# Kernel optimization log

Measured on AMD Instinct MI355X. Metric: run time of the kernel, lower is better.

## Reference

```python
import jax, jax.numpy as jnp
import numpy as np

B, N, C, H = 4, 1024, 256, 8
HD = C // H
SCALE = HD ** -0.5


def setup_inputs() -> dict:
    key = jax.random.key(0)
    ks = jax.random.split(key, 8)
    x = jax.random.normal(ks[0], (B, N, C), jnp.float32)
    voxel_coord = jax.random.uniform(ks[1], (B, N, 3), jnp.float32)
    # Linear weights stored as [in, out] so y = x @ W + b (same math as torch x @ W.T)
    W_qk = jax.random.normal(ks[2], (C, 2 * C), jnp.float32) * 0.02
    W_v = jax.random.normal(ks[3], (C, C), jnp.float32) * 0.02
    W_proj = jax.random.normal(ks[4], (C, C), jnp.float32) * 0.02
    b_proj = jnp.zeros((C,), jnp.float32)
    W_pos = jax.random.normal(ks[5], (4, H), jnp.float32) * 0.02
    b_pos = jnp.zeros((H,), jnp.float32)
    gating = jnp.ones((H,), jnp.float32)
    return dict(x=x, voxel_coord=voxel_coord, W_qk=W_qk, W_v=W_v,
                W_proj=W_proj, b_proj=b_proj, W_pos=W_pos, b_pos=b_pos,
                gating=gating)


def reference(x, voxel_coord, W_qk, W_v, W_proj, b_proj, W_pos, b_pos, gating):
    b, n, c = x.shape
    # Relative 3D positional encoding: positions[b,i,j] = p[j] - p[i]; feature = [dx,dy,dz,dist]
    diff = voxel_coord[:, None, :, :] - voxel_coord[:, :, None, :]          # [B,N,N,3]
    dist = jnp.sqrt(jnp.sum(diff * diff, axis=-1, keepdims=True))           # [B,N,N,1]
    rel = jnp.concatenate([diff, dist], axis=-1)                            # [B,N,N,4]

    # Positional score per head, softmax over keys j
    pos_logits = jnp.einsum('bijf,fh->bhij', rel, W_pos) + b_pos[None, :, None, None]
    pos_score = jax.nn.softmax(pos_logits, axis=-1)                         # [B,H,N,N]

    # Content score: SDPA with V = I  ==  plain softmax attention matrix
    qk = (x @ W_qk).reshape(b, n, 2, H, HD)
    q = jnp.transpose(qk[:, :, 0], (0, 2, 1, 3))                            # [B,H,N,hd]
    k = jnp.transpose(qk[:, :, 1], (0, 2, 1, 3))
    patch_score = jax.nn.softmax(jnp.einsum('bhid,bhjd->bhij', q, k) * SCALE, axis=-1)

    # Gated mix + renormalize
    sig = jax.nn.sigmoid(gating)[None, :, None, None]
    attn = (1.0 - sig) * patch_score + sig * pos_score
    attn = attn / jnp.sum(attn, axis=-1, keepdims=True)

    v = (x @ W_v).reshape(b, n, H, HD).transpose(0, 2, 1, 3)                # [B,H,N,hd]
    out = jnp.einsum('bhij,bhjd->bihd', attn, v).reshape(b, n, c)           # [B,N,C]
    out = out @ W_proj + b_proj
    return out
```

## Files before the change

### kernel.cpp

```cpp
#include <hip/hip_runtime.h>
#include <hip/hip_bf16.h>

#define LOG2E 1.4426950408889634f

typedef __attribute__((ext_vector_type(8))) short bf16x8_t;
typedef __attribute__((ext_vector_type(4))) float f32x4_t;

#if __has_builtin(__builtin_amdgcn_exp2f)
#define EXP2F_(x) __builtin_amdgcn_exp2f(x)
#else
__device__ __forceinline__ float EXP2F_(float x) {
    float r; asm volatile("v_exp_f32 %0, %1\ns_nop 1" : "=v"(r) : "v"(x)); return r;
}
#endif
#if __has_builtin(__builtin_amdgcn_sqrtf)
#define SQRTF_(x) __builtin_amdgcn_sqrtf(x)
#else
__device__ __forceinline__ float SQRTF_(float x) {
    float r; asm volatile("v_sqrt_f32 %0, %1\ns_nop 1" : "=v"(r) : "v"(x)); return r;
}
#endif

__device__ __forceinline__ unsigned short f2bf(float f) {
    unsigned u = __float_as_uint(f);
    u += 0x7fffu + ((u >> 16) & 1u);
    return (unsigned short)(u >> 16);
}

__device__ __forceinline__ unsigned pk2(float lo, float hi) {
    union { __hip_bfloat162 h2; unsigned u; } cvt;
    cvt.h2 = __float22bfloat162_rn(make_float2(lo, hi));
    return cvt.u;
}

__device__ __forceinline__ void stage16(const void* g, void* l, int lane) {
#if __has_builtin(__builtin_amdgcn_global_load_lds)
    __builtin_amdgcn_global_load_lds((const __attribute__((address_space(1))) void*)g,
                                     (__attribute__((address_space(3))) void*)l, 16, 0, 0);
#else
    *(uint4*)((char*)l + lane * 16) = *(const uint4*)g;
#endif
}

__global__ __launch_bounds__(256) void k_convert(
    const float* __restrict__ Wqk, const float* __restrict__ Wv,
    const float* __restrict__ Wpj, const float* __restrict__ coords,
    const float* __restrict__ W_pos,
    unsigned short* __restrict__ Wqk_t, unsigned short* __restrict__ Wv_t,
    unsigned short* __restrict__ Wp_t, float4* __restrict__ tbl)
{
    __shared__ unsigned short T[64 * 72];
    const int bid = blockIdx.x, tid = threadIdx.x;
    if (bid < 64) {
        const float* src; unsigned short* dst; int N_, kt, nt;
        if (bid < 32)      { src = Wqk; dst = Wqk_t; N_ = 512; kt = bid & 3; nt = bid >> 2; }
        else if (bid < 48) { int t = bid - 32; src = Wv;  dst = Wv_t; N_ = 256; kt = t & 3; nt = t >> 2; }
        else               { int t = bid - 48; src = Wpj; dst = Wp_t; N_ = 256; kt = t & 3; nt = t >> 2; }
        const int kr = tid >> 2, seg = tid & 3;
        #pragma unroll
        for (int u = 0; u < 4; ++u) {
            float4 v = *(const float4*)(src + (kt * 64 + kr) * N_ + nt * 64 + seg * 16 + u * 4);
            T[(seg * 16 + u * 4 + 0) * 72 + kr] = f2bf(v.x);
            T[(seg * 16 + u * 4 + 1) * 72 + kr] = f2bf(v.y);
            T[(seg * 16 + u * 4 + 2) * 72 + kr] = f2bf(v.z);
            T[(seg * 16 + u * 4 + 3) * 72 + kr] = f2bf(v.w);
        }
        __syncthreads();
        const int n = tid >> 2, s2 = tid & 3;
        uint4 a = *(uint4*)&T[n * 72 + s2 * 16];
        uint4 b2 = *(uint4*)&T[n * 72 + s2 * 16 + 8];
        *(uint4*)(dst + (nt * 64 + n) * 256 + kt * 64 + s2 * 16) = a;
        *(uint4*)(dst + (nt * 64 + n) * 256 + kt * 64 + s2 * 16 + 8) = b2;
    } else {
        const int bh = bid - 64, b = bh >> 3, h = bh & 7;
        const float wxl = W_pos[0 * 8 + h] * LOG2E;
        const float wyl = W_pos[1 * 8 + h] * LOG2E;
        const float wzl = W_pos[2 * 8 + h] * LOG2E;
        for (int jl = tid; jl < 1024; jl += 256) {
            float x = coords[(b * 1024 + jl) * 3 + 0];
            float y = coords[(b * 1024 + jl) * 3 + 1];
            float z = coords[(b * 1024 + jl) * 3 + 2];
            tbl[bh * 1024 + jl] = make_float4(x, y, z, fmaf(wxl, x, fmaf(wyl, y, wzl * z)));
        }
    }
}

__global__ __launch_bounds__(256) void k_qkv(
    const float* __restrict__ x,
    const unsigned short* __restrict__ Wqk_t,
    const unsigned short* __restrict__ Wv_t,
    unsigned short* __restrict__ q_ws, unsigned short* __restrict__ k_ws,
    unsigned short* __restrict__ v_ws)
{
    __shared__ unsigned short Al[64 * 64];
    __shared__ unsigned short Bl[64 * 64];
    const int tid = threadIdx.x;
    const int n0 = blockIdx.x * 64;
    const int row0 = blockIdx.y * 64;
    const int w = tid >> 6, lane = tid & 63;
    const int lhi = lane >> 4, llo = lane & 15;
    const unsigned short* Bsrc = (n0 < 512) ? (Wqk_t + n0 * 256) : (Wv_t + (n0 - 512) * 256);

    const int sr = lane >> 3, sc = lane & 7;
    const int scx = sc ^ sr;

    f32x4_t acc[4] = {};
    for (int kc = 0; kc < 4; ++kc) {
        #pragma unroll
        for (int s = 0; s < 2; ++s) {
            int chunk = w * 2 + s;
            int r = chunk * 8 + sr;
            const float* ax = x + (row0 + r) * 256 + kc * 64 + scx * 8;
            float4 a0 = *(const float4*)ax, a1 = *(const float4*)(ax + 4);
            uint4 pk;
            pk.x = pk2(a0.x, a0.y); pk.y = pk2(a0.z, a0.w);
            pk.z = pk2(a1.x, a1.y); pk.w = pk2(a1.z, a1.w);
            *(uint4*)(&Al[r * 64 + sc * 8]) = pk;
            stage16(Bsrc + r * 256 + kc * 64 + scx * 8, &Bl[chunk * 512], lane);
        }
        __syncthreads();
        #pragma unroll
        for (int ks = 0; ks < 2; ++ks) {
            int ua = ((ks * 4 + lhi) ^ (llo & 7)) * 8;
            bf16x8_t a = *(const bf16x8_t*)(&Al[(w * 16 + llo) * 64 + ua]);
            #pragma unroll
            for (int nt = 0; nt < 4; ++nt) {
                bf16x8_t b = *(const bf16x8_t*)(&Bl[(nt * 16 + llo) * 64 + ua]);
                acc[nt] = __builtin_amdgcn_mfma_f32_16x16x32_bf16(a, b, acc[nt], 0, 0, 0);
            }
        }
        __syncthreads();
    }
    constexpr float QSC = (float)(1.4426950408889634 / 5.656854249492380195206754896838);
    #pragma unroll
    for (int nt = 0; nt < 4; ++nt) {
        int ng = n0 + nt * 16 + llo;
        if (ng < 512) {
            #pragma unroll
            for (int r = 0; r < 4; ++r) {
                int ig = row0 + w * 16 + lhi * 4 + r;
                float val = acc[nt][r];
                int b = ig >> 10, i = ig & 1023;
                if (ng < 256) {
                    int h = ng >> 5, d = ng & 31;
                    q_ws[((b * 8 + h) * 1024 + i) * 32 + d] = f2bf(val * QSC);
                } else {
                    int c = ng - 256, h = c >> 5, d = c & 31;
                    k_ws[((b * 8 + h) * 1024 + i) * 32 + d] = f2bf(val);
                }
            }
        } else {
            int c = ng - 512, h = c >> 5, d = c & 31;
            int i0 = row0 + w * 16 + lhi * 4;
            int b = i0 >> 10, i = i0 & 1023;
            uint2 vv;
            vv.x = pk2(acc[nt][0], acc[nt][1]);
            vv.y = pk2(acc[nt][2], acc[nt][3]);
            *(uint2*)(v_ws + (size_t)(b * 8 + h) * 32768 + ((i >> 3) * 32 + d) * 8 + (i & 7)) = vv;
        }
    }
}

__global__ __launch_bounds__(512, 4) void k_attn(
    const unsigned short* __restrict__ q_ws,
    const unsigned short* __restrict__ k_ws,
    const unsigned short* __restrict__ v_ws,
    const float4* __restrict__ tbl,
    const float* __restrict__ W_pos,
    const float* __restrict__ b_pos,
    const float* __restrict__ gating,
    unsigned short* __restrict__ o_ws)
{
    __shared__ __align__(16) float4 TBL[1024];
    __shared__ __align__(16) unsigned short Wp[8 * 16 * 64];

    const int tid = threadIdx.x;
    const int bid = blockIdx.x;
    const int xcd = bid & 7, s = bid >> 3;
    const int bh = xcd * 4 + (s >> 4);
    const int it = s & 15;
    const int b = bh >> 3, h = bh & 7;

    const int w = tid >> 6, lane = tid & 63;
    const int wi = w & 3, wj = w >> 2;
    const int lhi = lane >> 4, llo = lane & 15;

    const float wdl = W_pos[3 * 8 + h] * LOG2E;
    const float bpl = b_pos[h] * LOG2E;

    const int i_base = it * 64 + wi * 16;
    bf16x8_t qf = *(const bf16x8_t*)(q_ws + (bh * 1024 + i_base + llo) * 32 + lhi * 8);

    const float4* tb4 = tbl + (size_t)bh * 1024;
    float4 icst = tb4[i_base + llo];
    const float xi = icst.x, yi = icst.y, zi = icst.z;
    const float cmb = bpl - icst.w;

    #pragma unroll
    for (int r = 0; r < 2; ++r) {
        int sidx = w * 128 + r * 64 + lane;
        stage16(tb4 + (sidx ^ ((sidx >> 3) & 7)), &TBL[w * 128 + r * 64], lane);
    }

    bf16x8_t ones;
    #pragma unroll
    for (int e = 0; e < 8; ++e) ones[e] = (short)0x3F80;

    f32x4_t accP[2] = {}, accQ[2] = {};
    f32x4_t accLp = {}, accLq = {};

    const unsigned short* kbase = k_ws + (size_t)bh * 32768;
    const unsigned short* vbase = v_ws + (size_t)bh * 32768;

    __syncthreads();

    for (int t = 0; t < 8; ++t) {
        const int j0 = wj * 512 + t * 64;
        bf16x8_t kf[4], vf[4];
        #pragma unroll
        for (int jq = 0; jq < 4; ++jq)
            kf[jq] = *(const bf16x8_t*)(kbase + (j0 + jq * 16 + llo) * 32 + lhi * 8);
        #pragma unroll
        for (int jb = 0; jb < 2; ++jb)
            #pragma unroll
            for (int dt = 0; dt < 2; ++dt)
                vf[jb * 2 + dt] = *(const bf16x8_t*)(vbase +
                    ((j0 + jb * 32 + lhi * 8) >> 3) * 256 + (dt * 16 + llo) * 8);

        bf16x8_t bQ[2];
        #pragma unroll
        for (int jb = 0; jb < 2; ++jb) {
            int jj = j0 + jb * 32 + lhi * 8;
            int xs = (jj >> 3) & 7;
            float eq[8];
            #pragma unroll
            for (int e = 0; e < 8; ++e) {
                float4 cj = TBL[jj + (e ^ xs)];
                float dx = cj.x - xi, dy = cj.y - yi, dz = cj.z - zi;
                float d2 = fmaf(dx, dx, fmaf(dy, dy, dz * dz));
                eq[e] = EXP2F_(fmaf(wdl, SQRTF_(d2), cj.w + cmb));
            }
            uint4 uq;
            uq.x = pk2(eq[0], eq[1]); uq.y = pk2(eq[2], eq[3]);
            uq.z = pk2(eq[4], eq[5]); uq.w = pk2(eq[6], eq[7]);
            bQ[jb] = *(bf16x8_t*)&uq;
        }

        #pragma unroll
        for (int jq = 0; jq < 4; ++jq) {
            f32x4_t zero = {};
            f32x4_t sv = __builtin_amdgcn_mfma_f32_16x16x32_bf16(kf[jq], qf, zero, 0, 0, 0);
            uint2 uP;
            uP.x = pk2(EXP2F_(sv[0]), EXP2F_(sv[1]));
            uP.y = pk2(EXP2F_(sv[2]), EXP2F_(sv[3]));
            int off = (w * 16 + llo) * 64 +
                      (((jq * 2 + (lhi >> 1)) ^ (llo & 7)) * 8) + (lhi & 1) * 4;
            *(uint2*)(&Wp[off]) = uP;
        }

        #pragma unroll
        for (int jb = 0; jb < 2; ++jb) {
            bf16x8_t bP = *(const bf16x8_t*)(&Wp[(w * 16 + llo) * 64 +
                                                 (((jb * 4 + lhi) ^ (llo & 7)) * 8)]);
            accLp = __builtin_amdgcn_mfma_f32_16x16x32_bf16(ones, bP, accLp, 0, 0, 0);
            accLq = __builtin_amdgcn_mfma_f32_16x16x32_bf16(ones, bQ[jb], accLq, 0, 0, 0);
            accP[0] = __builtin_amdgcn_mfma_f32_16x16x32_bf16(vf[jb * 2 + 0], bP, accP[0], 0, 0, 0);
            accP[1] = __builtin_amdgcn_mfma_f32_16x16x32_bf16(vf[jb * 2 + 1], bP, accP[1], 0, 0, 0);
            accQ[0] = __builtin_amdgcn_mfma_f32_16x16x32_bf16(vf[jb * 2 + 0], bQ[jb], accQ[0], 0, 0, 0);
            accQ[1] = __builtin_amdgcn_mfma_f32_16x16x32_bf16(vf[jb * 2 + 1], bQ[jb], accQ[1], 0, 0, 0);
        }
    }

    __syncthreads();
    float* red = (float*)Wp;
    float* LPQ = (float*)TBL;
    if (wj == 1) {
        float* pr = red + (wi * 64 + lane) * 16;
        *(f32x4_t*)(pr + 0) = accP[0]; *(f32x4_t*)(pr + 4)  = accP[1];
        *(f32x4_t*)(pr + 8) = accQ[0]; *(f32x4_t*)(pr + 12) = accQ[1];
        if (lhi == 0) { LPQ[wi * 16 + llo] = accLp[0]; LPQ[64 + wi * 16 + llo] = accLq[0]; }
    }
    __syncthreads();
    if (wj == 0) {
        const float* pr = red + (wi * 64 + lane) * 16;
        float Lp = accLp[0] + LPQ[wi * 16 + llo];
        float Lq = accLq[0] + LPQ[64 + wi * 16 + llo];
        float sig = 1.0f / (1.0f + __expf(-gating[h]));
        float ca = (1.0f - sig) / Lp, cb2 = sig / Lq;
        int rowg = b * 1024 + it * 64 + wi * 16 + llo;
        #pragma unroll
        for (int dt = 0; dt < 2; ++dt) {
            float o0 = ca * (accP[dt][0] + pr[dt * 4 + 0]) + cb2 * (accQ[dt][0] + pr[8 + dt * 4 + 0]);
            float o1 = ca * (accP[dt][1] + pr[dt * 4 + 1]) + cb2 * (accQ[dt][1] + pr[8 + dt * 4 + 1]);
            float o2 = ca * (accP[dt][2] + pr[dt * 4 + 2]) + cb2 * (accQ[dt][2] + pr[8 + dt * 4 + 2]);
            float o3 = ca * (accP[dt][3] + pr[dt * 4 + 3]) + cb2 * (accQ[dt][3] + pr[8 + dt * 4 + 3]);
            uint2 uu;
            uu.x = pk2(o0, o1); uu.y = pk2(o2, o3);
            *(uint2*)(o_ws + (size_t)rowg * 256 + h * 32 + dt * 16 + lhi * 4) = uu;
        }
    }
}

__global__ __launch_bounds__(256) void k_proj(
    const unsigned short* __restrict__ A,
    const unsigned short* __restrict__ Bt,
    const float* __restrict__ bias,
    float* __restrict__ out)
{
    __shared__ unsigned short Al[64 * 64];
    __shared__ unsigned short Bl[64 * 64];
    const int tid = threadIdx.x;
    const int n0 = blockIdx.x * 64;
    const int row0 = blockIdx.y * 64;
    const int w = tid >> 6, lane = tid & 63;
    const int lhi = lane >> 4, llo = lane & 15;
    const int sr = lane >> 3, sc = lane & 7;
    const int scx = sc ^ sr;

    f32x4_t acc[4] = {};
    for (int kc = 0; kc < 4; ++kc) {
        #pragma unroll
        for (int s = 0; s < 2; ++s) {
            int chunk = w * 2 + s;
            int r = chunk * 8 + sr;
            stage16(A + (row0 + r) * 256 + kc * 64 + scx * 8, &Al[chunk * 512], lane);
            stage16(Bt + (n0 + r) * 256 + kc * 64 + scx * 8, &Bl[chunk * 512], lane);
        }
        __syncthreads();
        #pragma unroll
        for (int ks = 0; ks < 2; ++ks) {
            int ua = ((ks * 4 + lhi) ^ (llo & 7)) * 8;
            bf16x8_t a = *(const bf16x8_t*)(&Al[(w * 16 + llo) * 64 + ua]);
            #pragma unroll
            for (int nt = 0; nt < 4; ++nt) {
                bf16x8_t b = *(const bf16x8_t*)(&Bl[(nt * 16 + llo) * 64 + ua]);
                acc[nt] = __builtin_amdgcn_mfma_f32_16x16x32_bf16(a, b, acc[nt], 0, 0, 0);
            }
        }
        __syncthreads();
    }
    #pragma unroll
    for (int nt = 0; nt < 4; ++nt) {
        int ng = n0 + nt * 16 + llo;
        float bv = bias[ng];
        #pragma unroll
        for (int r = 0; r < 4; ++r) {
            int ig = row0 + w * 16 + lhi * 4 + r;
            out[ig * 256 + ng] = acc[nt][r] + bv;
        }
    }
}

extern "C" void kernel_launch(void* const* d_in, const int* in_sizes, int n_in,
                              void* d_out, int out_size, void* d_ws, size_t ws_size,
                              hipStream_t stream)
{
    const float* x    = (const float*)d_in[0];
    const float* vc   = (const float*)d_in[1];
    const float* Wqk  = (const float*)d_in[2];
    const float* Wv   = (const float*)d_in[3];
    const float* Wpj  = (const float*)d_in[4];
    const float* bpj  = (const float*)d_in[5];
    const float* Wpos = (const float*)d_in[6];
    const float* bpos = (const float*)d_in[7];
    const float* gat  = (const float*)d_in[8];
    float* out = (float*)d_out;

    char* ws = (char*)d_ws;
    unsigned short* Wqk_t = (unsigned short*)(ws + 0);
    unsigned short* Wv_t  = (unsigned short*)(ws + 262144);
    unsigned short* Wp_t  = (unsigned short*)(ws + 393216);
    unsigned short* q_ws  = (unsigned short*)(ws + 524288);
    unsigned short* k_ws  = (unsigned short*)(ws + 2621440);
    unsigned short* v_ws  = (unsigned short*)(ws + 4718592);
    unsigned short* o_ws  = (unsigned short*)(ws + 6815744);
    float4*         tbl   = (float4*)(ws + 8912896);

    hipLaunchKernelGGL(k_convert, dim3(96), dim3(256), 0, stream,
                       Wqk, Wv, Wpj, vc, Wpos, Wqk_t, Wv_t, Wp_t, tbl);
    hipLaunchKernelGGL(k_qkv, dim3(12, 64), dim3(256), 0, stream,
                       x, Wqk_t, Wv_t, q_ws, k_ws, v_ws);
    hipLaunchKernelGGL(k_attn, dim3(512), dim3(512), 0, stream,
                       q_ws, k_ws, v_ws, tbl, Wpos, bpos, gat, o_ws);
    hipLaunchKernelGGL(k_proj, dim3(4, 64), dim3(256), 0, stream,
                       o_ws, Wp_t, bpj, out);
}
```

Before: 115.4 us.

## Compute pairwise squared distances and positional logits via split-bf16 MFMA

Moves the per-pair positional computation (squared distance and linear position logit) off scalar VALU and onto MFMA instructions. Coordinates are pre-split into hi/lo bf16 pairs in new per-key and per-query operand tables built by the convert kernel. The attention kernel drops the float4 coordinate table in LDS and adds a second LDS buffer to re-layout the positional exponentials for the PV MFMAs. This cuts VALU work in the inner loop but adds two MFMAs per 16-key slice, extra global loads for the A-operand table, and LDS round-trips. The expanded distance form can lose precision through cancellation, which the clamp to zero only partly covers. The b_pos term is dropped, which is valid only because it cancels in the softmax normalisation.

```diff
diff --git a/kernel.cpp b/kernel.cpp
--- a/kernel.cpp
+++ b/kernel.cpp
@@ -2,6 +2,7 @@
 #include <hip/hip_bf16.h>
 
 #define LOG2E 1.4426950408889634f
+#define ONEBF ((unsigned short)0x3F80)
 
 typedef __attribute__((ext_vector_type(8))) short bf16x8_t;
 typedef __attribute__((ext_vector_type(4))) float f32x4_t;
@@ -25,6 +26,12 @@
     unsigned u = __float_as_uint(f);
     u += 0x7fffu + ((u >> 16) & 1u);
     return (unsigned short)(u >> 16);
+}
+
+__device__ __forceinline__ void split2(float v, unsigned short& h, unsigned short& l) {
+    h = f2bf(v);
+    float fh = __uint_as_float((unsigned)h << 16);
+    l = f2bf(v - fh);
 }
 
 __device__ __forceinline__ unsigned pk2(float lo, float hi) {
@@ -47,7 +54,8 @@
     const float* __restrict__ Wpj, const float* __restrict__ coords,
     const float* __restrict__ W_pos,
     unsigned short* __restrict__ Wqk_t, unsigned short* __restrict__ Wv_t,
-    unsigned short* __restrict__ Wp_t, float4* __restrict__ tbl)
+    unsigned short* __restrict__ Wp_t,
+    unsigned short* __restrict__ AfT, unsigned short* __restrict__ BdT)
 {
     __shared__ unsigned short T[64 * 72];
     const int bid = blockIdx.x, tid = threadIdx.x;
@@ -71,16 +79,49 @@
         uint4 b2 = *(uint4*)&T[n * 72 + s2 * 16 + 8];
         *(uint4*)(dst + (nt * 64 + n) * 256 + kt * 64 + s2 * 16) = a;
         *(uint4*)(dst + (nt * 64 + n) * 256 + kt * 64 + s2 * 16 + 8) = b2;
-    } else {
+    } else if (bid < 96) {
         const int bh = bid - 64, b = bh >> 3, h = bh & 7;
         const float wxl = W_pos[0 * 8 + h] * LOG2E;
         const float wyl = W_pos[1 * 8 + h] * LOG2E;
         const float wzl = W_pos[2 * 8 + h] * LOG2E;
-        for (int jl = tid; jl < 1024; jl += 256) {
-            float x = coords[(b * 1024 + jl) * 3 + 0];
-            float y = coords[(b * 1024 + jl) * 3 + 1];
-            float z = coords[(b * 1024 + jl) * 3 + 2];
-            tbl[bh * 1024 + jl] = make_float4(x, y, z, fmaf(wxl, x, fmaf(wyl, y, wzl * z)));
+        const uint4 z = {0, 0, 0, 0};
+        for (int j = tid; j < 1024; j += 256) {
+            float x = coords[(b * 1024 + j) * 3 + 0];
+            float y = coords[(b * 1024 + j) * 3 + 1];
+            float z3 = coords[(b * 1024 + j) * 3 + 2];
+            float s = fmaf(x, x, fmaf(y, y, z3 * z3));
+            float a = fmaf(wzl, z3, fmaf(wyl, y, wxl * x));
+            unsigned short xh, xl, yh, yl, zh, zl, sh, sl, ah, al;
+            split2(x, xh, xl); split2(y, yh, yl); split2(z3, zh, zl);
+            split2(s, sh, sl); split2(a, ah, al);
+            unsigned short o[16] = { xh, xh, xl,  yh, yh, yl,  zh, zh, zl,
+                                     sh, sl, ONEBF,  ah, al, ONEBF, 0 };
+            unsigned short* blk = AfT + (size_t)bh * 32768 + (j >> 4) * 512;
+            *(uint4*)(blk + (j & 15) * 8)       = ((uint4*)o)[0];
+            *(uint4*)(blk + 128 + (j & 15) * 8) = ((uint4*)o)[1];
+            *(uint4*)(blk + 256 + (j & 15) * 8) = z;
+            *(uint4*)(blk + 384 + (j & 15) * 8) = z;
+        }
+    } else {
+        const int b = bid - 96;
+        const uint4 z = {0, 0, 0, 0};
+        for (int i = tid; i < 1024; i += 256) {
+            float x = coords[(b * 1024 + i) * 3 + 0];
+            float y = coords[(b * 1024 + i) * 3 + 1];
+            float z3 = coords[(b * 1024 + i) * 3 + 2];
+            float s = fmaf(x, x, fmaf(y, y, z3 * z3));
+            unsigned short m2xh, m2xl, m2yh, m2yl, m2zh, m2zl, sh, sl;
+            split2(-2.0f * x, m2xh, m2xl);
+            split2(-2.0f * y, m2yh, m2yl);
+            split2(-2.0f * z3, m2zh, m2zl);
+            split2(s, sh, sl);
+            unsigned short o[16] = { m2xh, m2xl, m2xh,  m2yh, m2yl, m2yh,  m2zh, m2zl, m2zh,
+                                     ONEBF, ONEBF, sh,  0, 0, sl, 0 };
+            unsigned short* blk = BdT + (size_t)b * 32768 + (i >> 4) * 512;
+            *(uint4*)(blk + (i & 15) * 8)       = ((uint4*)o)[0];
+            *(uint4*)(blk + 128 + (i & 15) * 8) = ((uint4*)o)[1];
+            *(uint4*)(blk + 256 + (i & 15) * 8) = z;
+            *(uint4*)(blk + 384 + (i & 15) * 8) = z;
         }
     }
 }
@@ -165,14 +206,14 @@
     const unsigned short* __restrict__ q_ws,
     const unsigned short* __restrict__ k_ws,
     const unsigned short* __restrict__ v_ws,
-    const float4* __restrict__ tbl,
+    const unsigned short* __restrict__ AfT,
+    const unsigned short* __restrict__ BdT,
     const float* __restrict__ W_pos,
-    const float* __restrict__ b_pos,
     const float* __restrict__ gating,
     unsigned short* __restrict__ o_ws)
 {
-    __shared__ __align__(16) float4 TBL[1024];
     __shared__ __align__(16) unsigned short Wp[8 * 16 * 64];
+    __shared__ __align__(16) unsigned short Wq[8 * 16 * 64];
 
     const int tid = threadIdx.x;
     const int bid = blockIdx.x;
@@ -186,21 +227,13 @@
     const int lhi = lane >> 4, llo = lane & 15;
 
     const float wdl = W_pos[3 * 8 + h] * LOG2E;
-    const float bpl = b_pos[h] * LOG2E;
 
     const int i_base = it * 64 + wi * 16;
     bf16x8_t qf = *(const bf16x8_t*)(q_ws + (bh * 1024 + i_base + llo) * 32 + lhi * 8);
-
-    const float4* tb4 = tbl + (size_t)bh * 1024;
-    float4 icst = tb4[i_base + llo];
-    const float xi = icst.x, yi = icst.y, zi = icst.z;
-    const float cmb = bpl - icst.w;
-
-    #pragma unroll
-    for (int r = 0; r < 2; ++r) {
-        int sidx = w * 128 + r * 64 + lane;
-        stage16(tb4 + (sidx ^ ((sidx >> 3) & 7)), &TBL[w * 128 + r * 64], lane);
-    }
+    bf16x8_t Bd2 = *(const bf16x8_t*)(BdT + (size_t)b * 32768 +
+                                      (it * 4 + wi) * 512 + (lhi * 16 + llo) * 8);
+    bf16x8_t Blin = {};
+    if (lhi == 1) { Blin[4] = (short)ONEBF; Blin[5] = (short)ONEBF; }
 
     bf16x8_t ones;
     #pragma unroll
@@ -211,40 +244,23 @@
 
     const unsigned short* kbase = k_ws + (size_t)bh * 32768;
     const unsigned short* vbase = v_ws + (size_t)bh * 32768;
-
-    __syncthreads();
+    const unsigned short* abase = AfT + (size_t)bh * 32768;
 
     for (int t = 0; t < 8; ++t) {
         const int j0 = wj * 512 + t * 64;
-        bf16x8_t kf[4], vf[4];
-        #pragma unroll
-        for (int jq = 0; jq < 4; ++jq)
+        bf16x8_t kf[4], af[4], vf[4];
+        #pragma unroll
+        for (int jq = 0; jq < 4; ++jq) {
             kf[jq] = *(const bf16x8_t*)(kbase + (j0 + jq * 16 + llo) * 32 + lhi * 8);
+            af[jq] = *(const bf16x8_t*)(abase + (wj * 32 + t * 4 + jq) * 512 +
+                                        (lhi * 16 + llo) * 8);
+        }
         #pragma unroll
         for (int jb = 0; jb < 2; ++jb)
             #pragma unroll
             for (int dt = 0; dt < 2; ++dt)
                 vf[jb * 2 + dt] = *(const bf16x8_t*)(vbase +
                     ((j0 + jb * 32 + lhi * 8) >> 3) * 256 + (dt * 16 + llo) * 8);
-
-        bf16x8_t bQ[2];
-        #pragma unroll
-        for (int jb = 0; jb < 2; ++jb) {
-            int jj = j0 + jb * 32 + lhi * 8;
-            int xs = (jj >> 3) & 7;
-            float eq[8];
-            #pragma unroll
-            for (int e = 0; e < 8; ++e) {
-                float4 cj = TBL[jj + (e ^ xs)];
-                float dx = cj.x - xi, dy = cj.y - yi, dz = cj.z - zi;
-                float d2 = fmaf(dx, dx, fmaf(dy, dy, dz * dz));
-                eq[e] = EXP2F_(fmaf(wdl, SQRTF_(d2), cj.w + cmb));
-            }
-            uint4 uq;
-            uq.x = pk2(eq[0], eq[1]); uq.y = pk2(eq[2], eq[3]);
-            uq.z = pk2(eq[4], eq[5]); uq.w = pk2(eq[6], eq[7]);
-            bQ[jb] = *(bf16x8_t*)&uq;
-        }
 
         #pragma unroll
         for (int jq = 0; jq < 4; ++jq) {
@@ -259,21 +275,39 @@
         }
 
         #pragma unroll
+        for (int jq = 0; jq < 4; ++jq) {
+            f32x4_t z1 = {}, z2 = {};
+            f32x4_t d2v = __builtin_amdgcn_mfma_f32_16x16x32_bf16(af[jq], Bd2, z1, 0, 0, 0);
+            f32x4_t lnv = __builtin_amdgcn_mfma_f32_16x16x32_bf16(af[jq], Blin, z2, 0, 0, 0);
+            float e0 = EXP2F_(fmaf(wdl, SQRTF_(fmaxf(d2v[0], 0.f)), lnv[0]));
+            float e1 = EXP2F_(fmaf(wdl, SQRTF_(fmaxf(d2v[1], 0.f)), lnv[1]));
+            float e2 = EXP2F_(fmaf(wdl, SQRTF_(fmaxf(d2v[2], 0.f)), lnv[2]));
+            float e3 = EXP2F_(fmaf(wdl, SQRTF_(fmaxf(d2v[3], 0.f)), lnv[3]));
+            uint2 uQ;
+            uQ.x = pk2(e0, e1);
+            uQ.y = pk2(e2, e3);
+            int off = (w * 16 + llo) * 64 +
+                      (((jq * 2 + (lhi >> 1)) ^ (llo & 7)) * 8) + (lhi & 1) * 4;
+            *(uint2*)(&Wq[off]) = uQ;
+        }
+
+        #pragma unroll
         for (int jb = 0; jb < 2; ++jb) {
-            bf16x8_t bP = *(const bf16x8_t*)(&Wp[(w * 16 + llo) * 64 +
-                                                 (((jb * 4 + lhi) ^ (llo & 7)) * 8)]);
+            int uu = ((jb * 4 + lhi) ^ (llo & 7)) * 8;
+            bf16x8_t bP = *(const bf16x8_t*)(&Wp[(w * 16 + llo) * 64 + uu]);
+            bf16x8_t bQ = *(const bf16x8_t*)(&Wq[(w * 16 + llo) * 64 + uu]);
             accLp = __builtin_amdgcn_mfma_f32_16x16x32_bf16(ones, bP, accLp, 0, 0, 0);
-            accLq = __builtin_amdgcn_mfma_f32_16x16x32_bf16(ones, bQ[jb], accLq, 0, 0, 0);
+            accLq = __builtin_amdgcn_mfma_f32_16x16x32_bf16(ones, bQ, accLq, 0, 0, 0);
             accP[0] = __builtin_amdgcn_mfma_f32_16x16x32_bf16(vf[jb * 2 + 0], bP, accP[0], 0, 0, 0);
             accP[1] = __builtin_amdgcn_mfma_f32_16x16x32_bf16(vf[jb * 2 + 1], bP, accP[1], 0, 0, 0);
-            accQ[0] = __builtin_amdgcn_mfma_f32_16x16x32_bf16(vf[jb * 2 + 0], bQ[jb], accQ[0], 0, 0, 0);
-            accQ[1] = __builtin_amdgcn_mfma_f32_16x16x32_bf16(vf[jb * 2 + 1], bQ[jb], accQ[1], 0, 0, 0);
+            accQ[0] = __builtin_amdgcn_mfma_f32_16x16x32_bf16(vf[jb * 2 + 0], bQ, accQ[0], 0, 0, 0);
+            accQ[1] = __builtin_amdgcn_mfma_f32_16x16x32_bf16(vf[jb * 2 + 1], bQ, accQ[1], 0, 0, 0);
         }
     }
 
     __syncthreads();
     float* red = (float*)Wp;
-    float* LPQ = (float*)TBL;
+    float* LPQ = (float*)Wq;
     if (wj == 1) {
         float* pr = red + (wi * 64 + lane) * 16;
         *(f32x4_t*)(pr + 0) = accP[0]; *(f32x4_t*)(pr + 4)  = accP[1];
@@ -365,6 +399,7 @@
     const float* bpos = (const float*)d_in[7];
     const float* gat  = (const float*)d_in[8];
     float* out = (float*)d_out;
+    (void)bpos;
 
     char* ws = (char*)d_ws;
     unsigned short* Wqk_t = (unsigned short*)(ws + 0);
@@ -374,14 +409,15 @@
     unsigned short* k_ws  = (unsigned short*)(ws + 2621440);
     unsigned short* v_ws  = (unsigned short*)(ws + 4718592);
     unsigned short* o_ws  = (unsigned short*)(ws + 6815744);
-    float4*         tbl   = (float4*)(ws + 8912896);
-
-    hipLaunchKernelGGL(k_convert, dim3(96), dim3(256), 0, stream,
-                       Wqk, Wv, Wpj, vc, Wpos, Wqk_t, Wv_t, Wp_t, tbl);
+    unsigned short* AfT   = (unsigned short*)(ws + 8912896);
+    unsigned short* BdT   = (unsigned short*)(ws + 11010048);
+
+    hipLaunchKernelGGL(k_convert, dim3(100), dim3(256), 0, stream,
+                       Wqk, Wv, Wpj, vc, Wpos, Wqk_t, Wv_t, Wp_t, AfT, BdT);
     hipLaunchKernelGGL(k_qkv, dim3(12, 64), dim3(256), 0, stream,
                        x, Wqk_t, Wv_t, q_ws, k_ws, v_ws);
     hipLaunchKernelGGL(k_attn, dim3(512), dim3(512), 0, stream,
-                       q_ws, k_ws, v_ws, tbl, Wpos, bpos, gat, o_ws);
+                       q_ws, k_ws, v_ws, AfT, BdT, Wpos, gat, o_ws);
     hipLaunchKernelGGL(k_proj, dim3(4, 64), dim3(256), 0, stream,
                        o_ws, Wp_t, bpj, out);
 }
```

New measurement: 109.7 us. -4.9%, faster.
